# Optimization experiments

Hardware: AMD Instinct MI355X
Metric: run time of the kernel (lower is better)

## Reference

```python
import jax, jax.numpy as jnp
import numpy as np

DIM = 1024
HEADS = 16
HEAD_DIM = DIM // HEADS
SCALE = float(HEAD_DIM ** (-0.25))
ROPE_BASE = 10000.0


def apply_rope(x):
    # x: [B, N, H, D], rotate-half RoPE over last dim
    B, N, H, D = x.shape
    half = D // 2
    inv_freq = 1.0 / (ROPE_BASE ** (jnp.arange(half, dtype=jnp.float32) / half))
    freqs = jnp.arange(N, dtype=jnp.float32)[:, None] * inv_freq[None, :]  # [N, half]
    cos = jnp.cos(freqs)[None, :, None, :].astype(x.dtype)  # [1,N,1,half]
    sin = jnp.sin(freqs)[None, :, None, :].astype(x.dtype)
    x1, x2 = x[..., :half], x[..., half:]
    return jnp.concatenate([x1 * cos - x2 * sin, x1 * sin + x2 * cos], axis=-1)


def setup_inputs() -> dict:
    key = jax.random.key(0)
    k1, k2, k3 = jax.random.split(key, 3)
    x = jax.random.normal(k1, (4, 4096, DIM), dtype=jnp.float32)
    w_qkv = jax.random.normal(k2, (DIM, 3 * DIM), dtype=jnp.float32) * 0.02
    w_out = jax.random.normal(k3, (DIM, DIM), dtype=jnp.float32) * 0.02
    return {"x": x, "w_qkv": w_qkv, "w_out": w_out}


def reference(x, w_qkv, w_out):
    B, N, D = x.shape
    qkv = x @ w_qkv  # [B, N, 3*D]
    q, k, v = jnp.split(qkv, 3, axis=-1)
    q = q.reshape(B, N, HEADS, HEAD_DIM)
    k = k.reshape(B, N, HEADS, HEAD_DIM)
    v = v.reshape(B, N, HEADS, HEAD_DIM)
    q = apply_rope(q)
    k = apply_rope(k)
    # ELU(x*scale) + 1 feature map (positive)
    q = jax.nn.elu(q * SCALE) + 1.0
    k = jax.nn.elu(k * SCALE) + 1.0

    # sequential linear-attention recurrence over tokens (lax.scan)
    qT = jnp.moveaxis(q, 1, 0)  # [N, B, H, D]
    kT = jnp.moveaxis(k, 1, 0)
    vT = jnp.moveaxis(v, 1, 0)

    kv0 = jnp.zeros((B, HEADS, HEAD_DIM, HEAD_DIM), dtype=q.dtype)
    ks0 = jnp.zeros((B, HEADS, HEAD_DIM), dtype=q.dtype)

    def step(carry, qkv_t):
        kv, ks = carry
        qt, kt, vt = qkv_t
        kv = kv + jnp.einsum('bhd,bhm->bhdm', kt, vt)
        ks = ks + kt
        denom = jnp.maximum(jnp.einsum('bhd,bhd->bh', qt, ks), 1e-6)
        out_t = jnp.einsum('bhd,bhdm->bhm', qt, kv) / denom[..., None]
        return (kv, ks), out_t

    _, outT = jax.lax.scan(step, (kv0, ks0), (qT, kT, vT))  # outT: [N, B, H, D]
    out = jnp.moveaxis(outT, 0, 1).reshape(B, N, D)
    return out @ w_out
```

## Files before the change

### kernel.cpp

```cpp
#include <hip/hip_runtime.h>
#include <math.h>

#define BATCH 4
#define SEQ   4096
#define DMODEL 1024
#define HEADS 16
#define HDIM  64
#define CHUNK 64
#define NCHUNK 64
#define NTOK  16384
#define QKVC  3072
#define SCALE_F 0.35355339059327373f
#define ROPE_K 0.4152410118609203f

typedef unsigned short u16;
typedef _Float16 f16;
typedef __attribute__((ext_vector_type(8))) f16 f16x8;
typedef __attribute__((ext_vector_type(4))) float f32x4;

__device__ __forceinline__ u16 f2h(float f) { f16 h = (f16)f; return *(u16*)&h; }
__device__ __forceinline__ float h2f(u16 u) { f16 h = *(f16*)&u; return (float)h; }
__device__ __forceinline__ void storeC(u16* p, float v) { *p = f2h(v); }
__device__ __forceinline__ void storeC(float* p, float v) { *p = v; }

__device__ __forceinline__ void gload_lds16(const u16* g, u16* l)
{
    __builtin_amdgcn_global_load_lds(
        (const __attribute__((address_space(1))) void*)g,
        (__attribute__((address_space(3))) void*)l, 16, 0, 0);
}

__global__ __launch_bounds__(256)
void convert_f32_f16(const float* __restrict__ src, u16* __restrict__ dst)
{
    long i = ((long)blockIdx.x * 256 + threadIdx.x) * 4;
    float4 v = *(const float4*)(src + i);
    ushort4 o; o.x = f2h(v.x); o.y = f2h(v.y); o.z = f2h(v.z); o.w = f2h(v.w);
    *(ushort4*)(dst + i) = o;
}

__global__ __launch_bounds__(256)
void transpose_convert(const float* __restrict__ src, int C,
                       u16* __restrict__ dst, int dld)
{
    __shared__ u16 tile[64][72];
    const int r0 = blockIdx.y * 64, c0 = blockIdx.x * 64;
    const int t = threadIdx.x;
    const int rr = t >> 4, cc4 = (t & 15) * 4;
#pragma unroll
    for (int j = 0; j < 4; ++j) {
        int r = rr + j * 16;
        float4 v = *(const float4*)(src + (long)(r0 + r) * C + c0 + cc4);
        tile[cc4 + 0][r] = f2h(v.x);
        tile[cc4 + 1][r] = f2h(v.y);
        tile[cc4 + 2][r] = f2h(v.z);
        tile[cc4 + 3][r] = f2h(v.w);
    }
    __syncthreads();
#pragma unroll
    for (int j = 0; j < 4; ++j) {
        int c = rr + j * 16;
        ushort4 o = *(ushort4*)&tile[c][cc4];
        *(ushort4*)(dst + (long)(c0 + c) * dld + r0 + cc4) = o;
    }
}

template <typename CT, bool ROPE>
__global__ __launch_bounds__(256)
void gemm_mfma(const u16* __restrict__ A, int lda,
               const u16* __restrict__ BT, int ldbt,
               CT* __restrict__ C, int ldc, int K)
{
    __shared__ u16 As[128][32];
    __shared__ u16 Bs[128][32];

    const int tid = threadIdx.x;
    const long m0 = blockIdx.y * 128, n0 = blockIdx.x * 128;
    const int w = tid >> 6, lane = tid & 63;
    const int wm = (w >> 1) * 64, wn = (w & 1) * 64;
    const int fr = lane & 15;
    const int fk = (lane >> 4) * 8;

    const int srow = w * 32 + (lane >> 2);
    const int scol = (lane & 3) * 8;
    const u16* ga = A  + (m0 + srow) * (long)lda  + scol;
    const u16* gb = BT + (n0 + srow) * (long)ldbt + scol;
    u16* const la = &As[w * 32][0];
    u16* const lb = &Bs[w * 32][0];
    const long astep = 16 * (long)lda;
    const long bstep = 16 * (long)ldbt;

    f32x4 acc[4][4];
#pragma unroll
    for (int i = 0; i < 4; ++i)
#pragma unroll
        for (int j = 0; j < 4; ++j)
#pragma unroll
            for (int r = 0; r < 4; ++r) acc[i][j][r] = 0.0f;

    for (int kt = 0; kt < K; kt += 32) {
        gload_lds16(ga,         la);
        gload_lds16(ga + astep, la + 16 * 32);
        gload_lds16(gb,         lb);
        gload_lds16(gb + bstep, lb + 16 * 32);
        ga += 32; gb += 32;
        __syncthreads();

        f16x8 af[4], bf[4];
#pragma unroll
        for (int i = 0; i < 4; ++i) {
            af[i] = *(const f16x8*)&As[wm + i * 16 + fr][fk];
            bf[i] = *(const f16x8*)&Bs[wn + i * 16 + fr][fk];
        }
#pragma unroll
        for (int i = 0; i < 4; ++i)
#pragma unroll
            for (int j = 0; j < 4; ++j)
                acc[i][j] = __builtin_amdgcn_mfma_f32_16x16x32_f16(af[i], bf[j], acc[i][j], 0, 0, 0);
        __syncthreads();
    }

    const long cm = m0 + wm + (lane >> 4) * 4;
    const long cn = n0 + wn + fr;

    if (ROPE && cn < 2048) {
        const float invf0 = exp2f(-(float)fr * ROPE_K);
        const float invf1 = exp2f(-(float)(fr + 16) * ROPE_K);
#pragma unroll
        for (int i = 0; i < 4; ++i)
#pragma unroll
            for (int r = 0; r < 4; ++r) {
                long row = cm + i * 16 + r;
                float n = (float)(int)(row & (SEQ - 1));
                float s0, c0, s1, c1;
                __sincosf(n * invf0, &s0, &c0);
                __sincosf(n * invf1, &s1, &c1);
                float x1 = acc[i][0][r], x2 = acc[i][2][r];
                float x3 = acc[i][1][r], x4 = acc[i][3][r];
                float u1 = (x1 * c0 - x2 * s0) * SCALE_F;
                float u2 = (x1 * s0 + x2 * c0) * SCALE_F;
                float u3 = (x3 * c1 - x4 * s1) * SCALE_F;
                float u4 = (x3 * s1 + x4 * c1) * SCALE_F;
                u1 = (u1 > 0.0f) ? (u1 + 1.0f) : __expf(u1);
                u2 = (u2 > 0.0f) ? (u2 + 1.0f) : __expf(u2);
                u3 = (u3 > 0.0f) ? (u3 + 1.0f) : __expf(u3);
                u4 = (u4 > 0.0f) ? (u4 + 1.0f) : __expf(u4);
                CT* pr = C + row * ldc + cn;
                storeC(pr, u1); storeC(pr + 16, u3);
                storeC(pr + 32, u2); storeC(pr + 48, u4);
            }
    } else {
#pragma unroll
        for (int i = 0; i < 4; ++i)
#pragma unroll
            for (int j = 0; j < 4; ++j)
#pragma unroll
                for (int r = 0; r < 4; ++r)
                    storeC(&C[(cm + i * 16 + r) * ldc + cn + j * 16], acc[i][j][r]);
    }
}

__global__ __launch_bounds__(256)
void chunk_sums_mfma(const u16* __restrict__ qkv,
                     u16* __restrict__ S, float* __restrict__ ksum)
{
    __shared__ u16 Kt[64][72];
    __shared__ u16 Vt[64][72];

    const int blk = blockIdx.x;
    const int c = blk & 63, bh = blk >> 6;
    const int b = bh >> 4, h = bh & 15;
    const int tid = threadIdx.x;
    const long base = (long)(b * SEQ + c * CHUNK) * QKVC + h * HDIM;

#pragma unroll
    for (int j = 0; j < 4; ++j) {
        int i4 = (j * 256 + tid) * 4;
        int t = i4 >> 6, d = i4 & 63;
        const u16* src = qkv + base + (long)t * QKVC + d;
        ushort4 kk = *(const ushort4*)(src + DMODEL);
        ushort4 vv = *(const ushort4*)(src + 2 * DMODEL);
        Kt[d + 0][t] = kk.x; Kt[d + 1][t] = kk.y;
        Kt[d + 2][t] = kk.z; Kt[d + 3][t] = kk.w;
        Vt[d + 0][t] = vv.x; Vt[d + 1][t] = vv.y;
        Vt[d + 2][t] = vv.z; Vt[d + 3][t] = vv.w;
    }
    __syncthreads();

    const int w = tid >> 6, lane = tid & 63;
    const int fr = lane & 15, quad = lane >> 4;

    f16x8 af0 = *(const f16x8*)&Vt[w * 16 + fr][quad * 8];
    f16x8 af1 = *(const f16x8*)&Vt[w * 16 + fr][32 + quad * 8];
    f32x4 acc[4];
#pragma unroll
    for (int j = 0; j < 4; ++j)
#pragma unroll
        for (int r = 0; r < 4; ++r) acc[j][r] = 0.0f;
#pragma unroll
    for (int j = 0; j < 4; ++j) {
        f16x8 b0 = *(const f16x8*)&Kt[j * 16 + fr][quad * 8];
        f16x8 b1 = *(const f16x8*)&Kt[j * 16 + fr][32 + quad * 8];
        acc[j] = __builtin_amdgcn_mfma_f32_16x16x32_f16(af0, b0, acc[j], 0, 0, 0);
        acc[j] = __builtin_amdgcn_mfma_f32_16x16x32_f16(af1, b1, acc[j], 0, 0, 0);
    }
    const long sb = (long)blk * 4096;
    const int mrow = w * 16 + quad * 4;
#pragma unroll
    for (int j = 0; j < 4; ++j)
#pragma unroll
        for (int r = 0; r < 4; ++r)
            S[sb + (mrow + r) * 64 + j * 16 + fr] = f2h(acc[j][r]);

    if (tid < 64) {
        float s = 0.0f;
        for (int t = 0; t < 64; ++t) s += h2f(Kt[tid][t]);
        ksum[(long)blk * 64 + tid] = s;
    }
}

__global__ __launch_bounds__(256)
void scan_kernel(u16* __restrict__ S, float* __restrict__ ksum)
{
    const int blk = blockIdx.x;
    const int slice = blk & 15, bh = blk >> 4;
    const int p = slice * 256 + threadIdx.x;
    const long base = (long)bh * NCHUNK * 4096 + p;
    float acc = 0.0f;
    for (int c = 0; c < NCHUNK; ++c) {
        long idx = base + (long)c * 4096;
        float tmp = h2f(S[idx]);
        S[idx] = f2h(acc);
        acc += tmp;
    }
    if (slice == 0 && threadIdx.x < 64) {
        const long kb = (long)bh * NCHUNK * 64 + threadIdx.x;
        float ka = 0.0f;
        for (int c = 0; c < NCHUNK; ++c) {
            float t = ksum[kb + (long)c * 64];
            ksum[kb + (long)c * 64] = ka;
            ka += t;
        }
    }
}

__global__ __launch_bounds__(256)
void chunk_out_mfma(u16* __restrict__ qkv,
                    const u16* __restrict__ S, const float* __restrict__ ksum)
{
    __shared__ u16 Qs[64][72];
    __shared__ u16 Ks[64][72];
    __shared__ u16 Vt[64][72];
    __shared__ u16 KVt[64][72];
    __shared__ u16 Sch[64][72];
    __shared__ float kss[64];
    __shared__ float den[64];

    const int blk = blockIdx.x;
    const int c = blk & 63, bh = blk >> 6;
    const int b = bh >> 4, h = bh & 15;
    const int tid = threadIdx.x;
    const long base = (long)(b * SEQ + c * CHUNK) * QKVC + h * HDIM;

#pragma unroll
    for (int j = 0; j < 4; ++j) {
        int i4 = (j * 256 + tid) * 4;
        int t = i4 >> 6, d = i4 & 63;
        const u16* src = qkv + base + (long)t * QKVC + d;
        *(ushort4*)&Qs[t][d] = *(const ushort4*)(src);
        *(ushort4*)&Ks[t][d] = *(const ushort4*)(src + DMODEL);
        ushort4 vv = *(const ushort4*)(src + 2 * DMODEL);
        Vt[d + 0][t] = vv.x; Vt[d + 1][t] = vv.y;
        Vt[d + 2][t] = vv.z; Vt[d + 3][t] = vv.w;
        *(ushort4*)&KVt[t][d] = *(const ushort4*)(S + (long)blk * 4096 + i4);
    }
    if (tid < 64) kss[tid] = ksum[(long)blk * 64 + tid];
    __syncthreads();

    const int w = tid >> 6, lane = tid & 63;
    const int fr = lane & 15, quad = lane >> 4;
    const int trow = w * 16 + quad * 4;

    f16x8 aq0 = *(const f16x8*)&Qs[w * 16 + fr][quad * 8];
    f16x8 aq1 = *(const f16x8*)&Qs[w * 16 + fr][32 + quad * 8];
    f32x4 sc[4];
#pragma unroll
    for (int j = 0; j < 4; ++j)
#pragma unroll
        for (int r = 0; r < 4; ++r) sc[j][r] = 0.0f;
#pragma unroll
    for (int j = 0; j < 4; ++j) {
        f16x8 b0 = *(const f16x8*)&Ks[j * 16 + fr][quad * 8];
        f16x8 b1 = *(const f16x8*)&Ks[j * 16 + fr][32 + quad * 8];
        sc[j] = __builtin_amdgcn_mfma_f32_16x16x32_f16(aq0, b0, sc[j], 0, 0, 0);
        sc[j] = __builtin_amdgcn_mfma_f32_16x16x32_f16(aq1, b1, sc[j], 0, 0, 0);
    }
#pragma unroll
    for (int j = 0; j < 4; ++j)
#pragma unroll
        for (int r = 0; r < 4; ++r) {
            int t = trow + r, s = j * 16 + fr;
            Sch[t][s] = f2h(s <= t ? sc[j][r] : 0.0f);
        }
    __syncthreads();

    if (tid < 64) {
        float dn = 0.0f;
        for (int d = 0; d < 64; ++d) dn += h2f(Qs[tid][d]) * kss[d];
        for (int s = 0; s <= tid; ++s) dn += h2f(Sch[tid][s]);
        den[tid] = 1.0f / fmaxf(dn, 1e-6f);
    }
    __syncthreads();

    f16x8 as0 = *(const f16x8*)&Sch[w * 16 + fr][quad * 8];
    f16x8 as1 = *(const f16x8*)&Sch[w * 16 + fr][32 + quad * 8];
    f32x4 oc[4];
#pragma unroll
    for (int j = 0; j < 4; ++j)
#pragma unroll
        for (int r = 0; r < 4; ++r) oc[j][r] = 0.0f;
#pragma unroll
    for (int j = 0; j < 4; ++j) {
        f16x8 b0 = *(const f16x8*)&Vt[j * 16 + fr][quad * 8];
        f16x8 b1 = *(const f16x8*)&Vt[j * 16 + fr][32 + quad * 8];
        oc[j] = __builtin_amdgcn_mfma_f32_16x16x32_f16(as0, b0, oc[j], 0, 0, 0);
        oc[j] = __builtin_amdgcn_mfma_f32_16x16x32_f16(as1, b1, oc[j], 0, 0, 0);
        f16x8 k0 = *(const f16x8*)&KVt[j * 16 + fr][quad * 8];
        f16x8 k1 = *(const f16x8*)&KVt[j * 16 + fr][32 + quad * 8];
        oc[j] = __builtin_amdgcn_mfma_f32_16x16x32_f16(aq0, k0, oc[j], 0, 0, 0);
        oc[j] = __builtin_amdgcn_mfma_f32_16x16x32_f16(aq1, k1, oc[j], 0, 0, 0);
    }
#pragma unroll
    for (int j = 0; j < 4; ++j)
#pragma unroll
        for (int r = 0; r < 4; ++r) {
            int t = trow + r;
            qkv[base + (long)t * QKVC + j * 16 + fr] = f2h(oc[j][r] * den[t]);
        }
}

extern "C" void kernel_launch(void* const* d_in, const int* in_sizes, int n_in,
                              void* d_out, int out_size, void* d_ws, size_t ws_size,
                              hipStream_t stream)
{
    const float* x     = (const float*)d_in[0];
    const float* w_qkv = (const float*)d_in[1];
    const float* w_out = (const float*)d_in[2];
    float* out = (float*)d_out;

    u16* qkv = (u16*)d_ws;
    u16* xf16  = (u16*)d_out;
    u16* wqkvT = xf16 + (size_t)NTOK * DMODEL;
    u16* S     = (u16*)d_out;
    float* ksum = (float*)((char*)d_out + 33554432);
    u16* woutT = qkv + 1024;

    dim3 blk(256);

    convert_f32_f16<<<NTOK * DMODEL / 1024, blk, 0, stream>>>(x, xf16);
    transpose_convert<<<dim3(QKVC / 64, DMODEL / 64), blk, 0, stream>>>(
        w_qkv, QKVC, wqkvT, DMODEL);

    gemm_mfma<u16, true><<<dim3(QKVC / 128, NTOK / 128), blk, 0, stream>>>(
        xf16, DMODEL, wqkvT, DMODEL, qkv, QKVC, DMODEL);

    chunk_sums_mfma<<<64 * NCHUNK, blk, 0, stream>>>(qkv, S, ksum);
    scan_kernel<<<64 * 16, blk, 0, stream>>>(S, ksum);
    chunk_out_mfma<<<64 * NCHUNK, blk, 0, stream>>>(qkv, S, ksum);

    transpose_convert<<<dim3(DMODEL / 64, DMODEL / 64), blk, 0, stream>>>(
        w_out, DMODEL, woutT, QKVC);
    gemm_mfma<float, false><<<dim3(DMODEL / 128, NTOK / 128), blk, 0, stream>>>(
        qkv, QKVC, woutT, QKVC, out, DMODEL, DMODEL);
}
```

Measured before the change: 415.8 us.

## Rewrite GEMM with 256x256 tiles, 4-stage LDS ring and swizzled layout

Result: faster. 380.7 us (-8.4%).

```diff
diff --git a/kernel.cpp b/kernel.cpp
--- a/kernel.cpp
+++ b/kernel.cpp
@@ -30,6 +30,16 @@
         (__attribute__((address_space(3))) void*)l, 16, 0, 0);
 }
 
+#define BAR_STAGE(N) \
+    asm volatile("s_waitcnt vmcnt(" #N ")" ::: "memory"); \
+    __builtin_amdgcn_s_barrier(); \
+    __builtin_amdgcn_sched_barrier(0);
+
+#define BAR_END() \
+    asm volatile("s_waitcnt lgkmcnt(0)" ::: "memory"); \
+    __builtin_amdgcn_s_barrier(); \
+    __builtin_amdgcn_sched_barrier(0);
+
 __global__ __launch_bounds__(256)
 void convert_f32_f16(const float* __restrict__ src, u16* __restrict__ dst)
 {
@@ -66,77 +76,95 @@
 }
 
 template <typename CT, bool ROPE>
-__global__ __launch_bounds__(256)
+__global__ __launch_bounds__(512, 2)
 void gemm_mfma(const u16* __restrict__ A, int lda,
                const u16* __restrict__ BT, int ldbt,
                CT* __restrict__ C, int ldc, int K)
 {
-    __shared__ u16 As[128][32];
-    __shared__ u16 Bs[128][32];
+    __shared__ u16 ringA[4][256 * 32];
+    __shared__ u16 ringB[4][256 * 32];
 
     const int tid = threadIdx.x;
-    const long m0 = blockIdx.y * 128, n0 = blockIdx.x * 128;
+    const long m0 = (long)blockIdx.y * 256, n0 = (long)blockIdx.x * 256;
     const int w = tid >> 6, lane = tid & 63;
-    const int wm = (w >> 1) * 64, wn = (w & 1) * 64;
-    const int fr = lane & 15;
-    const int fk = (lane >> 4) * 8;
-
-    const int srow = w * 32 + (lane >> 2);
-    const int scol = (lane & 3) * 8;
+    const int wm = w >> 2, wn = w & 3;
+    const int fr = lane & 15, quad = lane >> 4;
+    const int sw = (quad ^ ((fr >> 1) & 3)) * 8;
+
+    const int srow = tid >> 2;
+    const int scol = ((tid & 3) ^ ((tid >> 3) & 3)) * 8;
     const u16* ga = A  + (m0 + srow) * (long)lda  + scol;
     const u16* gb = BT + (n0 + srow) * (long)ldbt + scol;
-    u16* const la = &As[w * 32][0];
-    u16* const lb = &Bs[w * 32][0];
-    const long astep = 16 * (long)lda;
-    const long bstep = 16 * (long)ldbt;
-
-    f32x4 acc[4][4];
-#pragma unroll
-    for (int i = 0; i < 4; ++i)
+    const long a128 = 128 * (long)lda, b128 = 128 * (long)ldbt;
+
+    f32x4 acc[8][4];
+#pragma unroll
+    for (int i = 0; i < 8; ++i)
 #pragma unroll
         for (int j = 0; j < 4; ++j)
 #pragma unroll
             for (int r = 0; r < 4; ++r) acc[i][j][r] = 0.0f;
 
-    for (int kt = 0; kt < K; kt += 32) {
-        gload_lds16(ga,         la);
-        gload_lds16(ga + astep, la + 16 * 32);
-        gload_lds16(gb,         lb);
-        gload_lds16(gb + bstep, lb + 16 * 32);
-        ga += 32; gb += 32;
-        __syncthreads();
-
-        f16x8 af[4], bf[4];
-#pragma unroll
-        for (int i = 0; i < 4; ++i) {
-            af[i] = *(const f16x8*)&As[wm + i * 16 + fr][fk];
-            bf[i] = *(const f16x8*)&Bs[wn + i * 16 + fr][fk];
-        }
-#pragma unroll
-        for (int i = 0; i < 4; ++i)
-#pragma unroll
-            for (int j = 0; j < 4; ++j)
-                acc[i][j] = __builtin_amdgcn_mfma_f32_16x16x32_f16(af[i], bf[j], acc[i][j], 0, 0, 0);
-        __syncthreads();
-    }
-
-    const long cm = m0 + wm + (lane >> 4) * 4;
-    const long cn = n0 + wn + fr;
+    auto STAGE = [&](int h) {
+        const int s = h & 3;
+        u16* la = &ringA[s][w * 512];
+        u16* lb = &ringB[s][w * 512];
+        const long ko = (long)h << 5;
+        gload_lds16(ga + ko,        la);
+        gload_lds16(ga + ko + a128, la + 4096);
+        gload_lds16(gb + ko,        lb);
+        gload_lds16(gb + ko + b128, lb + 4096);
+    };
+
+    auto COMPUTE = [&](int h) {
+        const u16* As_ = ringA[h & 3];
+        const u16* Bs_ = ringB[h & 3];
+        f16x8 af[8], bf[4];
+#pragma unroll
+        for (int mi = 0; mi < 8; ++mi)
+            af[mi] = *(const f16x8*)&As_[(wm * 128 + mi * 16 + fr) * 32 + sw];
+#pragma unroll
+        for (int nj = 0; nj < 4; ++nj)
+            bf[nj] = *(const f16x8*)&Bs_[(wn * 64 + nj * 16 + fr) * 32 + sw];
+        __builtin_amdgcn_s_setprio(1);
+#pragma unroll
+        for (int mi = 0; mi < 8; ++mi)
+#pragma unroll
+            for (int nj = 0; nj < 4; ++nj)
+                acc[mi][nj] = __builtin_amdgcn_mfma_f32_16x16x32_f16(
+                    af[mi], bf[nj], acc[mi][nj], 0, 0, 0);
+        __builtin_amdgcn_s_setprio(0);
+    };
+
+    const int NH = K >> 5;
+    STAGE(0); STAGE(1); STAGE(2);
+    for (int h = 0; h < NH - 3; ++h) {
+        STAGE(h + 3);
+        BAR_STAGE(12);
+        COMPUTE(h);
+        BAR_END();
+    }
+    BAR_STAGE(8);  COMPUTE(NH - 3);
+    BAR_STAGE(4);  COMPUTE(NH - 2);
+    BAR_STAGE(0);  COMPUTE(NH - 1);
+
+    const long cm = m0 + wm * 128 + quad * 4;
+    const long cn = n0 + wn * 64 + fr;
 
     if (ROPE && cn < 2048) {
         const float invf0 = exp2f(-(float)fr * ROPE_K);
         const float invf1 = exp2f(-(float)(fr + 16) * ROPE_K);
 #pragma unroll
-        for (int i = 0; i < 4; ++i)
+        for (int mi = 0; mi < 8; ++mi)
 #pragma unroll
             for (int r = 0; r < 4; ++r) {
-                long row = cm + i * 16 + r;
+                long row = cm + mi * 16 + r;
                 float n = (float)(int)(row & (SEQ - 1));
                 float s0, c0, s1, c1;
                 __sincosf(n * invf0, &s0, &c0);
                 __sincosf(n * invf1, &s1, &c1);
-                float x1 = acc[i][0][r], x2 = acc[i][2][r];
-                float x3 = acc[i][1][r], x4 = acc[i][3][r];
+                float x1 = acc[mi][0][r], x2 = acc[mi][2][r];
+                float x3 = acc[mi][1][r], x4 = acc[mi][3][r];
                 float u1 = (x1 * c0 - x2 * s0) * SCALE_F;
                 float u2 = (x1 * s0 + x2 * c0) * SCALE_F;
                 float u3 = (x3 * c1 - x4 * s1) * SCALE_F;
@@ -151,12 +179,12 @@
             }
     } else {
 #pragma unroll
-        for (int i = 0; i < 4; ++i)
-#pragma unroll
-            for (int j = 0; j < 4; ++j)
+        for (int mi = 0; mi < 8; ++mi)
+#pragma unroll
+            for (int nj = 0; nj < 4; ++nj)
 #pragma unroll
                 for (int r = 0; r < 4; ++r)
-                    storeC(&C[(cm + i * 16 + r) * ldc + cn + j * 16], acc[i][j][r]);
+                    storeC(&C[(cm + mi * 16 + r) * ldc + cn + nj * 16], acc[mi][nj][r]);
     }
 }
 
@@ -356,12 +384,13 @@
     u16* woutT = qkv + 1024;
 
     dim3 blk(256);
+    dim3 gblk(512);
 
     convert_f32_f16<<<NTOK * DMODEL / 1024, blk, 0, stream>>>(x, xf16);
     transpose_convert<<<dim3(QKVC / 64, DMODEL / 64), blk, 0, stream>>>(
         w_qkv, QKVC, wqkvT, DMODEL);
 
-    gemm_mfma<u16, true><<<dim3(QKVC / 128, NTOK / 128), blk, 0, stream>>>(
+    gemm_mfma<u16, true><<<dim3(QKVC / 256, NTOK / 256), gblk, 0, stream>>>(
         xf16, DMODEL, wqkvT, DMODEL, qkv, QKVC, DMODEL);
 
     chunk_sums_mfma<<<64 * NCHUNK, blk, 0, stream>>>(qkv, S, ksum);
@@ -370,6 +399,6 @@
 
     transpose_convert<<<dim3(DMODEL / 64, DMODEL / 64), blk, 0, stream>>>(
         w_out, DMODEL, woutT, QKVC);
-    gemm_mfma<float, false><<<dim3(DMODEL / 128, NTOK / 128), blk, 0, stream>>>(
+    gemm_mfma<float, false><<<dim3(DMODEL / 256, NTOK / 256), gblk, 0, stream>>>(
         qkv, QKVC, woutT, QKVC, out, DMODEL, DMODEL);
 }
```
